# Optimization experiments

Hardware: AMD Instinct MI355X
Metric: run time of the kernel (lower is better)

The kernel has to match this reference:

```python
import jax, jax.numpy as jnp
import numpy as np
import math

B = 2
LAYERS = 18
LATENT = 512
MAPPER_LAYER = 7  # w_code_num[attention_layer=11]
CLUSTERS = 10
CLUSTER_LAYER = 11
CLUSTER_DIM = 512 + 2 * (512 // 16)  # 576
LR_MUL = 0.1
LAYER_NUM = [0, 2, 3, 5, 6, 8, 9, 11, 12, 14, 15, 17, 18, 20, 21, 23, 24]
CH = [512] * 11 + [256] * 2 + [128] * 3 + [64] * 3 + [32] * 3 + [16] * 3
RES = [4, 8, 8, 16, 16, 32, 32, 64, 64, 128, 128] + [256] * 14


def _forward(x, fmaps, mw, mb, afw, afb, aw, ab, alw, alb, initial_state):
    batch = x.shape[0]
    blend = fmaps[CLUSTER_LAYER - 1]
    size = blend.shape[2]  # 128

    # ---- cluster assignment (torch.no_grad block) ----
    pc = blend.shape[1] // 16  # position_channel = 32
    coords = jnp.arange(size, dtype=jnp.float32) * (2.0 / (size - 1)) - 1.0
    xp = jnp.broadcast_to(coords[None, :], (size, size))
    yp = jnp.broadcast_to(coords[:, None], (size, size))
    cf = jnp.concatenate([
        blend,
        jnp.broadcast_to(xp[None, None], (batch, pc, size, size)),
        jnp.broadcast_to(yp[None, None], (batch, pc, size, size)),
    ], axis=1)
    cf = jax.lax.stop_gradient(cf)
    flat = cf.transpose(0, 2, 3, 1).reshape(-1, cf.shape[1])  # [B*S*S, 576]
    dis = (jnp.sum(flat * flat, axis=1, keepdims=True)
           - 2.0 * flat @ initial_state.T
           + jnp.sum(initial_state * initial_state, axis=1)[None, :])
    assign = jnp.argmin(dis, axis=1).reshape(batch, size, size)
    choice = jnp.arange(batch)[:, None, None] * CLUSTERS + assign  # [B,S,S]

    x7 = x[:, :MAPPER_LAYER, -LATENT:]
    h = x7 * jax.lax.rsqrt(jnp.mean(x7 * x7, axis=-1, keepdims=True) + 1e-8)
    w_scale = (1.0 / math.sqrt(LATENT)) * LR_MUL
    for i in range(3):
        h = jnp.einsum('bci,coi->bco', h, mw[:, i]) * w_scale
        h = jax.nn.leaky_relu(h + mb[:, i][None] * LR_MUL, 0.2) * math.sqrt(2.0)
    delta_zs = jnp.concatenate(
        [h, jnp.zeros((batch, LAYERS - MAPPER_LAYER, LATENT), h.dtype)], axis=1)
    loss_delta = jnp.mean(jnp.sqrt(jnp.sum(delta_zs[:, :MAPPER_LAYER] ** 2, axis=-1)))

    # ---- attention branch (EqualConv2d 1x1 + nearest interpolate, torch semantics) ----
    def conv1x1(f, w, b):
        cin = f.shape[1]
        return jnp.einsum('bihw,oi->bohw', f, w) * (1.0 / math.sqrt(cin)) + b[None, :, None, None]

    def interp(f):  # torch nearest: src = floor(i * in / out)
        H = f.shape[2]
        idx = (jnp.arange(size) * H) // size
        return f[:, :, idx][:, :, :, idx]

    att = [interp(conv1x1(fmaps[-1], afw, afb))]
    for c in range(LAYERS - 1):
        f = fmaps[LAYER_NUM[c]]
        att.append(interp(conv1x1(f, aw[c][:, :f.shape[1]], ab[c])))
    amap = jnp.concatenate(att, axis=1)  # [B, 32*18, S, S]
    logits = jnp.einsum('bihw,i->bhw', amap, alw) * (1.0 / math.sqrt(32 * LAYERS)) + alb[0]
    each = jax.nn.sigmoid(logits)  # [B,S,S]

    # ---- training branch: per-(batch,cluster) masked mean -> segment mean ----
    nseg = batch * CLUSTERS
    seg = choice.reshape(-1)
    vals = each.reshape(-1)
    sums = jax.ops.segment_sum(vals, seg, num_segments=nseg)
    cnts = jax.ops.segment_sum(jnp.ones_like(vals), seg, num_segments=nseg)
    mean = sums / jnp.maximum(cnts, 1.0)
    attention_map = jnp.where(cnts > 0, mean, 1.0)[choice]  # [B,S,S]
    loss_reg = jnp.sum(jnp.where(cnts > 0, jnp.maximum(mean - 0.8, 0.0), 0.0)) / batch
    loss_tv = jnp.mean((each - jax.lax.stop_gradient(attention_map)) ** 2)

    am = attention_map[:, None]  # [B,1,S,S]
    final = jnp.where(am < 0.8, am - jax.lax.stop_gradient(am), am)
    # torchvision gaussian_blur(k=5): sigma = 0.3*((5-1)*0.5-1)+0.8 = 1.1, reflect pad
    xs = jnp.linspace(-2.0, 2.0, 5)
    k1 = jnp.exp(-0.5 * (xs / 1.1) ** 2)
    k1 = k1 / jnp.sum(k1)
    k2 = jnp.outer(k1, k1)[None, None]  # [1,1,5,5]
    padded = jnp.pad(final, ((0, 0), (0, 0), (2, 2), (2, 2)), mode='reflect')
    blurred = jax.lax.conv_general_dilated(padded, k2.astype(final.dtype), (1, 1), 'VALID')
    return delta_zs, blurred, loss_delta, loss_reg, loss_tv


def setup_inputs() -> dict:
    key = jax.random.key(0)
    ks = jax.random.split(key, 40)
    inp = {}
    inp['x'] = jax.random.normal(ks[0], (B, LAYERS, LATENT), jnp.float32)
    for i in range(25):
        inp[f'fmap_{i}'] = jax.random.normal(ks[1 + i], (B, CH[i], RES[i], RES[i]), jnp.float32)
    inp['fmap_25'] = jax.random.normal(ks[26], (B, 512, 4, 4), jnp.float32)
    inp['mw'] = jax.random.normal(ks[27], (MAPPER_LAYER, 3, LATENT, LATENT), jnp.float32)
    inp['mb'] = 0.1 * jax.random.normal(ks[28], (MAPPER_LAYER, 3, LATENT), jnp.float32)
    inp['afw'] = jax.random.normal(ks[29], (32, 512), jnp.float32)
    inp['afb'] = 0.1 * jax.random.normal(ks[30], (32,), jnp.float32)
    inp['aw'] = jax.random.normal(ks[31], (LAYERS - 1, 32, 512), jnp.float32)
    inp['ab'] = 0.1 * jax.random.normal(ks[32], (LAYERS - 1, 32), jnp.float32)
    inp['alw'] = jax.random.normal(ks[33], (32 * LAYERS,), jnp.float32)
    inp['alb'] = jnp.full((1,), 5.0, jnp.float32)  # attention_last bias init to 5
    inp['initial_state'] = jax.random.normal(ks[34], (CLUSTERS, CLUSTER_DIM), jnp.float32)
    inp['size'] = 128
    return inp


def reference(x, fmap_0, fmap_1, fmap_2, fmap_3, fmap_4, fmap_5, fmap_6, fmap_7,
              fmap_8, fmap_9, fmap_10, fmap_11, fmap_12, fmap_13, fmap_14, fmap_15,
              fmap_16, fmap_17, fmap_18, fmap_19, fmap_20, fmap_21, fmap_22, fmap_23,
              fmap_24, fmap_25, mw, mb, afw, afb, aw, ab, alw, alb, initial_state, size):
    fmaps = [fmap_0, fmap_1, fmap_2, fmap_3, fmap_4, fmap_5, fmap_6, fmap_7, fmap_8,
             fmap_9, fmap_10, fmap_11, fmap_12, fmap_13, fmap_14, fmap_15, fmap_16,
             fmap_17, fmap_18, fmap_19, fmap_20, fmap_21, fmap_22, fmap_23, fmap_24,
             fmap_25]
    return _forward(x, fmaps, mw, mb, afw, afb, aw, ab, alw, alb, initial_state)
```

## Files before the change

### kernel.cpp

```cpp
#include <hip/hip_runtime.h>
#include <math.h>

#define NPIX 32768
#define OUT_DZ 0
#define OUT_BLUR 18432
#define OUT_LD 51200
#define OUT_REG 51201
#define OUT_TV 51202

__constant__ int d_cin[18] = {512,512,512,512,512,512,512,512,256,256,128,128,64,64,32,32,16,16};
__constant__ int d_H[18]   = {4,  4,  8,  16, 32, 32, 64, 128,256,256,256,256,256,256,256,256,256,256};

struct FPtrs { const float* f[18]; };

#define WS_HA     0
#define WS_HB     7168
#define WS_ST     14336
#define WS_CN     22528
#define WS_BIASP  22576
#define WS_V      22656
#define WS_CHOICE 31872
#define WS_PART   64640
#define WS_EACH   654464
#define WS_SUMS   687232
#define WS_CNTS   689792
#define WS_ATTV   692352
#define WS_TVP    692384

#define WAITVM(N) asm volatile("s_waitcnt vmcnt(" #N ")" ::: "memory")

__global__ __launch_bounds__(512) void k_pre(
    const float* __restrict__ afw, const float* __restrict__ afb,
    const float* __restrict__ aw,  const float* __restrict__ ab,
    const float* __restrict__ alw, const float* __restrict__ istate,
    float* __restrict__ v, float* __restrict__ biasp,
    float* __restrict__ st, float* __restrict__ cn,
    const float* __restrict__ x, float* __restrict__ h, float* __restrict__ out)
{
    __shared__ float red[512];
    __shared__ float scale;
    int bid = blockIdx.x;
    int tid = threadIdx.x;
    if (bid == 19 && tid == 0) out[OUT_TV] = 0.0f;
    if (bid < 18) {
        int t = bid;
        int cin = d_cin[t];
        const float* w  = (t==0) ? afw : aw + (size_t)(t-1)*32*512;
        const float* bb = (t==0) ? afb : ab + (t-1)*32;
        float sc = (1.0f/sqrtf((float)cin)) * (1.0f/24.0f);
        if (tid < cin) {
            float s = 0.0f;
            #pragma unroll 8
            for (int o = 0; o < 32; o++) s += alw[t*32+o] * w[o*512 + tid];
            v[t*512 + tid] = s * sc;
        }
        if (tid == 0) {
            float s = 0.0f;
            for (int o = 0; o < 32; o++) s += alw[t*32+o] * bb[o];
            biasp[t] = s * (1.0f/24.0f);
        }
    } else if (bid == 18) {
        if (tid < 512) {
            #pragma unroll
            for (int j = 0; j < 10; j++) st[tid*16 + j] = -2.0f * istate[j*576 + tid];
        }
        if (tid < 10) {
            int j = tid;
            float n = 0.0f, s1 = 0.0f, s2 = 0.0f;
            for (int k = 0; k < 576; k++) { float sv = istate[j*576+k]; n += sv*sv; }
            for (int k = 512; k < 544; k++) s1 += istate[j*576+k];
            for (int k = 544; k < 576; k++) s2 += istate[j*576+k];
            cn[j] = n; cn[16+j] = -2.0f*s1; cn[32+j] = -2.0f*s2;
        }
    } else {
        int r = bid - 19;
        int b = r / 7, c = r % 7;
        const float* xr = x + ((size_t)b*18 + c)*512;
        float v0 = xr[tid];
        red[tid] = v0*v0; __syncthreads();
        for (int s = 256; s; s >>= 1) { if (tid < s) red[tid] += red[tid+s]; __syncthreads(); }
        if (tid == 0) scale = 1.0f / sqrtf(red[0]*(1.0f/512.0f) + 1e-8f);
        __syncthreads();
        h[r*512 + tid] = v0*scale;
    }
}

__global__ __launch_bounds__(256) void k_mlp(
    const float* __restrict__ mw, const float* __restrict__ mb,
    const float* __restrict__ hin, float* __restrict__ hout,
    int layer, float* __restrict__ dz)
{
    int wave = blockIdx.x*4 + (threadIdx.x >> 6);
    int lane = threadIdx.x & 63;
    int c = wave >> 9, o = wave & 511;
    const float* wrow = mw + (((size_t)(c*3 + layer)*512 + o) << 9) + lane*8;
    float4 w0 = *(const float4*)wrow;
    float4 w1 = *(const float4*)(wrow + 4);
    const float* h0 = hin + (size_t)c*512 + lane*8;
    const float* h1 = hin + (size_t)(7 + c)*512 + lane*8;
    float4 a0 = *(const float4*)h0, a1 = *(const float4*)(h0+4);
    float4 b0 = *(const float4*)h1, b1 = *(const float4*)(h1+4);
    float d0 = a0.x*w0.x + a0.y*w0.y + a0.z*w0.z + a0.w*w0.w
             + a1.x*w1.x + a1.y*w1.y + a1.z*w1.z + a1.w*w1.w;
    float d1 = b0.x*w0.x + b0.y*w0.y + b0.z*w0.z + b0.w*w0.w
             + b1.x*w1.x + b1.y*w1.y + b1.z*w1.z + b1.w*w1.w;
    #pragma unroll
    for (int m = 32; m; m >>= 1) { d0 += __shfl_xor(d0, m); d1 += __shfl_xor(d1, m); }
    if (lane == 0) {
        const float wsc = (float)(0.1/22.62741699796952);
        const float rt2 = 1.41421356237309515f;
        float bias = mb[(c*3 + layer)*512 + o] * 0.1f;
        float z0 = d0*wsc + bias; z0 = (z0 > 0.0f ? z0 : 0.2f*z0) * rt2;
        float z1 = d1*wsc + bias; z1 = (z1 > 0.0f ? z1 : 0.2f*z1) * rt2;
        hout[(size_t)c*512 + o] = z0;
        hout[(size_t)(7 + c)*512 + o] = z1;
        if (dz) {
            dz[((size_t)0*18 + c)*512 + o] = z0;
            dz[((size_t)1*18 + c)*512 + o] = z1;
        }
    }
}

__global__ __launch_bounds__(256) void k_mega(FPtrs fp, const float* __restrict__ v,
    const float* __restrict__ blend, const float* __restrict__ st,
    const float* __restrict__ cn, int* __restrict__ choice,
    float* __restrict__ partial, const float* __restrict__ hB, float* __restrict__ out)
{
    __shared__ float smem[16896];
    int bid = blockIdx.x;
    int tid = threadIdx.x;

    if (bid < 2368) {
        int mk = bid / 37, mr = bid % 37;
        if (mr < 22) {
            int hid = mk*22 + mr;
            float (*buf)[4096] = (float(*)[4096])smem;
            float* vsh = smem + 16384;
            int t, b, rblk;
            if (hid < 128) { t = 7; b = hid >> 6; rblk = hid & 63; }
            else { int idx = hid - 128; t = 8 + (idx >> 7); int sub = idx & 127; b = sub >> 6; rblk = sub & 63; }
            int ch = d_cin[t];
            int H  = d_H[t];
            int y0 = rblk*2;
            int w = tid >> 6, lane = tid & 63;
            const float* base = fp.f[t] + (size_t)b*ch*(size_t)H*H;
            for (int i = tid; i < ch; i += 256) vsh[i] = v[t*512 + i];
            __syncthreads();

            int NP = (H == 128) ? (ch >> 4) : (ch >> 3);
            int S = (NP < 3) ? NP : 3;
            for (int q = 0; q < S; q++) {
                if (H == 256) {
                    #pragma unroll
                    for (int k = 0; k < 2; k++) {
                        int cl = 2*w + k;
                        const float* srcc = base + (size_t)(q*8 + cl)*65536 + (size_t)(2*y0)*256 + lane*4;
                        __builtin_amdgcn_global_load_lds(srcc,       &buf[q][(cl*2    )*256], 16, 0, 0);
                        __builtin_amdgcn_global_load_lds(srcc + 512, &buf[q][(cl*2 + 1)*256], 16, 0, 0);
                    }
                } else {
                    #pragma unroll
                    for (int k = 0; k < 4; k++) {
                        int cl = 4*w + k;
                        const float* srcc = base + (size_t)(q*16 + cl)*16384 + (size_t)y0*128 + lane*4;
                        __builtin_amdgcn_global_load_lds(srcc, &buf[q][cl*256], 16, 0, 0);
                    }
                }
            }
            int r = tid >> 7, x = tid & 127;
            float acc = 0.0f;
            for (int p = 0; p < NP; p++) {
                int ahead = S - p - 1;
                if (ahead >= 2)      { WAITVM(8); }
                else if (ahead == 1) { WAITVM(4); }
                else                 { WAITVM(0); }
                __builtin_amdgcn_sched_barrier(0);
                __builtin_amdgcn_s_barrier();
                __builtin_amdgcn_sched_barrier(0);
                if (S < NP) {
                    int q = S & 3;
                    if (H == 256) {
                        #pragma unroll
                        for (int k = 0; k < 2; k++) {
                            int cl = 2*w + k;
                            const float* srcc = base + (size_t)(S*8 + cl)*65536 + (size_t)(2*y0)*256 + lane*4;
                            __builtin_amdgcn_global_load_lds(srcc,       &buf[q][(cl*2    )*256], 16, 0, 0);
                            __builtin_amdgcn_global_load_lds(srcc + 512, &buf[q][(cl*2 + 1)*256], 16, 0, 0);
                        }
                    } else {
                        #pragma unroll
                        for (int k = 0; k < 4; k++) {
                            int cl = 4*w + k;
                            const float* srcc = base + (size_t)(S*16 + cl)*16384 + (size_t)y0*128 + lane*4;
                            __builtin_amdgcn_global_load_lds(srcc, &buf[q][cl*256], 16, 0, 0);
                        }
                    }
                    S++;
                }
                __builtin_amdgcn_sched_barrier(0);
                const float* bp = buf[p & 3];
                if (H == 256) {
                    int cb = p*8;
                    #pragma unroll
                    for (int cp = 0; cp < 8; cp++)
                        acc = fmaf(bp[(cp*2 + r)*256 + 2*x], vsh[cb + cp], acc);
                } else {
                    int cb = p*16;
                    #pragma unroll
                    for (int cp = 0; cp < 16; cp++)
                        acc = fmaf(bp[cp*256 + r*128 + x], vsh[cb + cp], acc);
                }
            }
            partial[(size_t)t*NPIX + b*16384 + (size_t)(y0 + r)*128 + x] = acc;
        } else if (mr < 30) {
            int aid = mk*8 + (mr - 22);
            float* gsh = smem;
            int csub = __builtin_amdgcn_readfirstlane(tid >> 6);
            int pl = tid & 63;
            int p = aid*64 + pl;
            int b = p >> 14, rem = p & 16383;
            float g[10] = {0,0,0,0,0,0,0,0,0,0};
            const float* src = blend + ((size_t)b*512 + csub*128)*16384 + rem;
            const float* stc = st + csub*128*16;
            for (int c0 = 0; c0 < 128; c0 += 8) {
                float q[8];
                #pragma unroll
                for (int u = 0; u < 8; u++) q[u] = src[(size_t)(c0+u) << 14];
                #pragma unroll
                for (int u = 0; u < 8; u++) {
                    #pragma unroll
                    for (int j = 0; j < 10; j++) g[j] = fmaf(q[u], stc[(c0+u)*16 + j], g[j]);
                }
            }
            #pragma unroll
            for (int j = 0; j < 10; j++) gsh[tid*10 + j] = g[j];
            __syncthreads();
            if (tid < 64) {
                int pp = aid*64 + tid;
                int bb = pp >> 14, rr = pp & 16383, y = rr >> 7, x = rr & 127;
                float cx = (float)x * (float)(2.0/127.0) - 1.0f;
                float cy = (float)y * (float)(2.0/127.0) - 1.0f;
                float gt[10];
                #pragma unroll
                for (int j = 0; j < 10; j++) {
                    gt[j] = cn[j] + cn[16+j]*cx + cn[32+j]*cy
                          + gsh[tid*10 + j] + gsh[(64+tid)*10 + j]
                          + gsh[(128+tid)*10 + j] + gsh[(192+tid)*10 + j];
                }
                int best = 0; float bg = gt[0];
                #pragma unroll
                for (int j = 1; j < 10; j++) if (gt[j] < bg) { bg = gt[j]; best = j; }
                choice[pp] = bb*10 + best;
            }
        } else {
            int lid = mk*7 + (mr - 30);
            float* vsh = smem;
            int t  = lid >> 6;
            int nc = d_cin[t];
            int H  = d_H[t];
            for (int i = tid; i < nc; i += 256) vsh[i] = v[t*512 + i];
            __syncthreads();
            int w = tid >> 6, lane = tid & 63;
            int px = lid & 63;
            int pbase = px*512;
            int b = pbase >> 14;
            int y = ((pbase & 16383) >> 7) + w;
            const float* base = fp.f[t] + (size_t)b*nc*(size_t)(H*H);
            float a0 = 0.0f, a1 = 0.0f;
            if (H == 64) {
                const float* src = base + (size_t)(y >> 1)*64 + lane;
                for (int cc = 0; cc < nc; cc += 8) {
                    float q[8];
                    #pragma unroll
                    for (int u = 0; u < 8; u++) q[u] = src[(size_t)(cc+u)*4096];
                    #pragma unroll
                    for (int u = 0; u < 8; u++) {
                        float vv = vsh[cc+u];
                        a0 = fmaf(q[u], vv, a0); a1 = fmaf(q[u], vv, a1);
                    }
                }
            } else {
                int x0 = 2*lane, x1 = 2*lane + 1;
                int sy = (y*H) >> 7, sx0 = (x0*H) >> 7, sx1 = (x1*H) >> 7;
                const float* src = base + (size_t)sy*H;
                size_t HH = (size_t)H*H;
                for (int cc = 0; cc < nc; cc += 8) {
                    float q0[8], q1[8];
                    #pragma unroll
                    for (int u = 0; u < 8; u++) {
                        q0[u] = src[(size_t)(cc+u)*HH + sx0];
                        q1[u] = src[(size_t)(cc+u)*HH + sx1];
                    }
                    #pragma unroll
                    for (int u = 0; u < 8; u++) {
                        float vv = vsh[cc+u];
                        a0 = fmaf(q0[u], vv, a0); a1 = fmaf(q1[u], vv, a1);
                    }
                }
            }
            int p = pbase + w*128 + 2*lane;
            float2 o; o.x = a0; o.y = a1;
            *(float2*)(partial + (size_t)t*NPIX + p) = o;
        }
    } else if (bid < 2412) {
        int z = (bid - 2368)*256 + tid;
        if (z < 11264) {
            int b = z / (11*512), rem = z % (11*512);
            out[(size_t)b*18*512 + 7*512 + rem] = 0.0f;
        }
    } else {
        float total = 0.0f;
        for (int r = 0; r < 14; r++) {
            float v0 = hB[r*512 + tid], v1 = hB[r*512 + 256 + tid];
            smem[tid] = v0*v0 + v1*v1; __syncthreads();
            for (int s = 128; s; s >>= 1) { if (tid < s) smem[tid] += smem[tid+s]; __syncthreads(); }
            if (tid == 0) total += sqrtf(smem[0]);
            __syncthreads();
        }
        if (tid == 0) out[OUT_LD] = total * (1.0f/14.0f);
    }
}

__global__ __launch_bounds__(256) void k_logits(
    const float* __restrict__ partial, const float* __restrict__ biasp,
    const float* __restrict__ alb, const int* __restrict__ choice,
    float* __restrict__ each, float* __restrict__ bsums, int* __restrict__ bcnts)
{
    __shared__ float ssum[20]; __shared__ int scnt[20]; __shared__ float sbias;
    int tid = threadIdx.x;
    if (tid < 20) { ssum[tid] = 0.0f; scnt[tid] = 0; }
    if (tid == 0) {
        float s = alb[0];
        for (int t = 0; t < 18; t++) s += biasp[t];
        sbias = s;
    }
    __syncthreads();
    int p = blockIdx.x*256 + tid;
    float lg = sbias;
    #pragma unroll
    for (int s = 0; s < 18; s++) lg += partial[(size_t)s*NPIX + p];
    float e = 1.0f / (1.0f + expf(-lg));
    each[p] = e;
    int ch = choice[p];
    atomicAdd(&ssum[ch], e);
    atomicAdd(&scnt[ch], 1);
    __syncthreads();
    if (tid < 20) { bsums[blockIdx.x*20 + tid] = ssum[tid]; bcnts[blockIdx.x*20 + tid] = scnt[tid]; }
}

__global__ __launch_bounds__(256) void k_final(
    const float* __restrict__ each, const int* __restrict__ choice,
    const float* __restrict__ bsums, const int* __restrict__ bcnts,
    float* __restrict__ out)
{
    __shared__ float av[20];
    __shared__ float regsh[20];
    __shared__ float red[256];
    int tid = threadIdx.x;
    if (tid < 20) {
        float s = 0.0f; int c = 0;
        for (int blk = 0; blk < 128; blk++) { s += bsums[blk*20 + tid]; c += bcnts[blk*20 + tid]; }
        float mean = s / fmaxf((float)c, 1.0f);
        av[tid] = (c > 0) ? mean : 1.0f;
        regsh[tid] = (c > 0) ? fmaxf(mean - 0.8f, 0.0f) : 0.0f;
    }
    __syncthreads();
    if (blockIdx.x == 0 && tid == 0) {
        float rs = 0.0f;
        for (int j = 0; j < 20; j++) rs += regsh[j];
        out[OUT_REG] = rs * 0.5f;
    }
    int p = blockIdx.x*256 + tid;
    int b = p >> 14, rem = p & 16383, y = rem >> 7, x = rem & 127;
    float k1[5]; float ks = 0.0f;
    #pragma unroll
    for (int i = 0; i < 5; i++) { float d = (float)(i-2) / 1.1f; k1[i] = expf(-0.5f*d*d); ks += k1[i]; }
    #pragma unroll
    for (int i = 0; i < 5; i++) k1[i] /= ks;
    const int* cb = choice + b*16384;
    float acc = 0.0f;
    #pragma unroll
    for (int a = 0; a < 5; a++) {
        int yy = y + a - 2; yy = (yy < 0) ? -yy : ((yy > 127) ? 254 - yy : yy);
        #pragma unroll
        for (int bb = 0; bb < 5; bb++) {
            int xx = x + bb - 2; xx = (xx < 0) ? -xx : ((xx > 127) ? 254 - xx : xx);
            float am = av[cb[yy*128 + xx]];
            float fin = (am < 0.8f) ? 0.0f : am;
            acc += k1[a]*k1[bb]*fin;
        }
    }
    out[OUT_BLUR + p] = acc;
    float amc = av[cb[y*128 + x]];
    float d = each[p] - amc;
    red[tid] = d*d; __syncthreads();
    for (int s = 128; s; s >>= 1) { if (tid < s) red[tid] += red[tid+s]; __syncthreads(); }
    if (tid == 0) atomicAdd(&out[OUT_TV], red[0] * (1.0f/32768.0f));
}

extern "C" void kernel_launch(void* const* d_in, const int* in_sizes, int n_in,
                              void* d_out, int out_size, void* d_ws, size_t ws_size,
                              hipStream_t stream)
{
    const float* x      = (const float*)d_in[0];
    const float* blend  = (const float*)d_in[11];
    const float* mw     = (const float*)d_in[27];
    const float* mb     = (const float*)d_in[28];
    const float* afw    = (const float*)d_in[29];
    const float* afb    = (const float*)d_in[30];
    const float* aw     = (const float*)d_in[31];
    const float* ab     = (const float*)d_in[32];
    const float* alw    = (const float*)d_in[33];
    const float* alb    = (const float*)d_in[34];
    const float* istate = (const float*)d_in[35];
    float* out = (float*)d_out;
    float* ws  = (float*)d_ws;

    static const int LN[17] = {0,2,3,5,6,8,9,11,12,14,15,17,18,20,21,23,24};
    FPtrs fp;
    fp.f[0] = (const float*)d_in[26];
    for (int c = 0; c < 17; c++) fp.f[1+c] = (const float*)d_in[1 + LN[c]];

    float* hA     = ws + WS_HA;
    float* hB     = ws + WS_HB;
    float* st     = ws + WS_ST;
    float* cn     = ws + WS_CN;
    float* biasp  = ws + WS_BIASP;
    float* v      = ws + WS_V;
    int*   choice = (int*)(ws + WS_CHOICE);
    float* part   = ws + WS_PART;
    float* each   = ws + WS_EACH;
    float* bsums  = ws + WS_SUMS;
    int*   bcnts  = (int*)(ws + WS_CNTS);

    k_pre<<<33, 512, 0, stream>>>(afw, afb, aw, ab, alw, istate, v, biasp, st, cn, x, hA, out);
    k_mlp<<<896, 256, 0, stream>>>(mw, mb, hA, hB, 0, nullptr);
    k_mlp<<<896, 256, 0, stream>>>(mw, mb, hB, hA, 1, nullptr);
    k_mlp<<<896, 256, 0, stream>>>(mw, mb, hA, hB, 2, out + OUT_DZ);
    k_mega<<<2413, 256, 0, stream>>>(fp, v, blend, st, cn, choice, part, hB, out);
    k_logits<<<128, 256, 0, stream>>>(part, biasp, alb, choice, each, bsums, bcnts);
    k_final<<<128, 256, 0, stream>>>(each, choice, bsums, bcnts, out);
}
```

Measured before the change: 139.2 us.

## Restructure cluster-assignment blocks to stream full channels via async LDS pipeline

The cluster-assignment role in the mega kernel is rewritten. Before, each block covered 64 pixels with channels split across four waves and reduced through shared memory. Now each block owns 256 pixels (two rows) and streams all 512 channels through a 4-deep global_load_lds ring buffer, with cluster-state weights staged in LDS, so the cross-wave reduction disappears. The number of assignment blocks per group falls from 8 to 2, which shrinks the grid and makes each block longer, so load balance and occupancy could shift.

```diff
diff --git a/kernel.cpp b/kernel.cpp
--- a/kernel.cpp
+++ b/kernel.cpp
@@ -24,8 +24,6 @@
 #define WS_EACH   654464
 #define WS_SUMS   687232
 #define WS_CNTS   689792
-#define WS_ATTV   692352
-#define WS_TVP    692384
 
 #define WAITVM(N) asm volatile("s_waitcnt vmcnt(" #N ")" ::: "memory")
 
@@ -130,8 +128,8 @@
     int bid = blockIdx.x;
     int tid = threadIdx.x;
 
-    if (bid < 2368) {
-        int mk = bid / 37, mr = bid % 37;
+    if (bid < 1984) {
+        int mk = bid / 31, mr = bid % 31;
         if (mr < 22) {
             int hid = mk*22 + mr;
             float (*buf)[4096] = (float(*)[4096])smem;
@@ -212,48 +210,73 @@
                 }
             }
             partial[(size_t)t*NPIX + b*16384 + (size_t)(y0 + r)*128 + x] = acc;
-        } else if (mr < 30) {
-            int aid = mk*8 + (mr - 22);
-            float* gsh = smem;
-            int csub = __builtin_amdgcn_readfirstlane(tid >> 6);
-            int pl = tid & 63;
-            int p = aid*64 + pl;
-            int b = p >> 14, rem = p & 16383;
+        } else if (mr < 24) {
+            int aid = mk*2 + (mr - 22);
+            float (*buf)[2048] = (float(*)[2048])smem;
+            float* stsh = smem + 8192;
+            int b  = aid >> 6;
+            int y0 = (aid & 63)*2;
+            int w = tid >> 6, lane = tid & 63;
+            const float* base = blend + (size_t)b*512*16384 + (size_t)y0*128;
+            for (int i = tid; i < 5120; i += 256) {
+                int c = i / 10, j = i - c*10;
+                stsh[i] = st[c*16 + j];
+            }
+            __syncthreads();
+            const int NP = 64;
+            int S = 3;
+            for (int q = 0; q < S; q++) {
+                #pragma unroll
+                for (int k = 0; k < 2; k++) {
+                    int cl = 2*w + k;
+                    const float* srcc = base + (size_t)(q*8 + cl)*16384 + lane*4;
+                    __builtin_amdgcn_global_load_lds(srcc, &buf[q][cl*256], 16, 0, 0);
+                }
+            }
             float g[10] = {0,0,0,0,0,0,0,0,0,0};
-            const float* src = blend + ((size_t)b*512 + csub*128)*16384 + rem;
-            const float* stc = st + csub*128*16;
-            for (int c0 = 0; c0 < 128; c0 += 8) {
-                float q[8];
+            for (int p = 0; p < NP; p++) {
+                int ahead = S - p - 1;
+                if (ahead >= 2)      { WAITVM(4); }
+                else if (ahead == 1) { WAITVM(2); }
+                else                 { WAITVM(0); }
+                __builtin_amdgcn_sched_barrier(0);
+                __builtin_amdgcn_s_barrier();
+                __builtin_amdgcn_sched_barrier(0);
+                if (S < NP) {
+                    int q = S & 3;
+                    #pragma unroll
+                    for (int k = 0; k < 2; k++) {
+                        int cl = 2*w + k;
+                        const float* srcc = base + (size_t)(S*8 + cl)*16384 + lane*4;
+                        __builtin_amdgcn_global_load_lds(srcc, &buf[q][cl*256], 16, 0, 0);
+                    }
+                    S++;
+                }
+                __builtin_amdgcn_sched_barrier(0);
+                const float* bp = buf[p & 3];
+                int cb = p*8;
                 #pragma unroll
-                for (int u = 0; u < 8; u++) q[u] = src[(size_t)(c0+u) << 14];
-                #pragma unroll
-                for (int u = 0; u < 8; u++) {
-                    #pragma unroll
-                    for (int j = 0; j < 10; j++) g[j] = fmaf(q[u], stc[(c0+u)*16 + j], g[j]);
-                }
-            }
+                for (int cl = 0; cl < 8; cl++) {
+                    float q = bp[cl*256 + tid];
+                    const float* sr = &stsh[(cb + cl)*10];
+                    #pragma unroll
+                    for (int j = 0; j < 10; j++) g[j] = fmaf(q, sr[j], g[j]);
+                }
+            }
+            int r = tid >> 7, x = tid & 127;
+            int y = y0 + r;
+            float cx = (float)x * (float)(2.0/127.0) - 1.0f;
+            float cy = (float)y * (float)(2.0/127.0) - 1.0f;
+            int best = 0;
+            float bg = g[0] + cn[0] + cn[16]*cx + cn[32]*cy;
             #pragma unroll
-            for (int j = 0; j < 10; j++) gsh[tid*10 + j] = g[j];
-            __syncthreads();
-            if (tid < 64) {
-                int pp = aid*64 + tid;
-                int bb = pp >> 14, rr = pp & 16383, y = rr >> 7, x = rr & 127;
-                float cx = (float)x * (float)(2.0/127.0) - 1.0f;
-                float cy = (float)y * (float)(2.0/127.0) - 1.0f;
-                float gt[10];
-                #pragma unroll
-                for (int j = 0; j < 10; j++) {
-                    gt[j] = cn[j] + cn[16+j]*cx + cn[32+j]*cy
-                          + gsh[tid*10 + j] + gsh[(64+tid)*10 + j]
-                          + gsh[(128+tid)*10 + j] + gsh[(192+tid)*10 + j];
-                }
-                int best = 0; float bg = gt[0];
-                #pragma unroll
-                for (int j = 1; j < 10; j++) if (gt[j] < bg) { bg = gt[j]; best = j; }
-                choice[pp] = bb*10 + best;
-            }
+            for (int j = 1; j < 10; j++) {
+                float gt = g[j] + cn[j] + cn[16+j]*cx + cn[32+j]*cy;
+                if (gt < bg) { bg = gt; best = j; }
+            }
+            choice[aid*256 + tid] = b*10 + best;
         } else {
-            int lid = mk*7 + (mr - 30);
+            int lid = mk*7 + (mr - 24);
             float* vsh = smem;
             int t  = lid >> 6;
             int nc = d_cin[t];
@@ -302,8 +325,8 @@
             float2 o; o.x = a0; o.y = a1;
             *(float2*)(partial + (size_t)t*NPIX + p) = o;
         }
-    } else if (bid < 2412) {
-        int z = (bid - 2368)*256 + tid;
+    } else if (bid < 2028) {
+        int z = (bid - 1984)*256 + tid;
         if (z < 11264) {
             int b = z / (11*512), rem = z % (11*512);
             out[(size_t)b*18*512 + 7*512 + rem] = 0.0f;
@@ -437,7 +460,7 @@
     k_mlp<<<896, 256, 0, stream>>>(mw, mb, hA, hB, 0, nullptr);
     k_mlp<<<896, 256, 0, stream>>>(mw, mb, hB, hA, 1, nullptr);
     k_mlp<<<896, 256, 0, stream>>>(mw, mb, hA, hB, 2, out + OUT_DZ);
-    k_mega<<<2413, 256, 0, stream>>>(fp, v, blend, st, cn, choice, part, hB, out);
+    k_mega<<<2029, 256, 0, stream>>>(fp, v, blend, st, cn, choice, part, hB, out);
     k_logits<<<128, 256, 0, stream>>>(part, biasp, alb, choice, each, bsums, bcnts);
     k_final<<<128, 256, 0, stream>>>(each, choice, bsums, bcnts, out);
 }
```

Result: no change. 138.1 us (-0.8%).
